# Performance work log

Measured on AMD Instinct MI355X. Metric: run time of the kernel, lower is better.

The kernel has to match this reference:

```python
import jax, jax.numpy as jnp
import numpy as np

N = 4096
IN_F = 256
OUT_F = 64
K = 4
ALPHA = 0.2  # LeakyReLU negative slope
NEG_INF = -9e15


def setup_inputs() -> dict:
    key = jax.random.key(0)
    k_h, k_w, k_a, k_e, k_m = jax.random.split(key, 5)
    h = jax.random.normal(k_h, (N, IN_F), dtype=jnp.float32)
    # xavier_uniform with gain=1.414
    def xavier(k, shape, gain=1.414):
        fan_in, fan_out = shape[0], shape[1]
        limit = gain * np.sqrt(6.0 / (fan_in + fan_out))
        return jax.random.uniform(k, shape, jnp.float32, -limit, limit)
    W = xavier(k_w, (IN_F, OUT_F))
    a = xavier(k_a, (2 * OUT_F, 1))
    vals = jax.random.uniform(k_e, (K, N, N), dtype=jnp.float32)
    mask = jax.random.uniform(k_m, (K, N, N), dtype=jnp.float32) < 0.05
    edge_attr = jnp.where(mask, vals, 0.0)
    return {"h": h, "edge_attr": edge_attr, "W": W, "a": a}


def reference(h, edge_attr, W, a):
    # h: [N, IN_F], edge_attr: [K, N, N], W: [IN_F, OUT_F], a: [2*OUT_F, 1]
    Wh = h @ W                                   # [N, OUT_F]
    Wh1 = Wh @ a[:OUT_F, :]                      # [N, 1]
    Wh2 = Wh @ a[OUT_F:, :]                      # [N, 1]
    e = jax.nn.leaky_relu(Wh1 + Wh2.T, negative_slope=ALPHA)  # [N, N]
    e = e[None, :, :] * edge_attr                # [K, N, N]
    e = jnp.where(edge_attr > 0, e, NEG_INF)
    att = jax.nn.softmax(e, axis=1)              # softmax over dim=1, as in torch
    # dropout is identity in eval mode
    # batched replacement for the per-channel python loop of matmuls
    hp = jnp.einsum('kij,jf->kif', att, Wh)      # [K, N, OUT_F]
    out = jnp.transpose(hp, (1, 0, 2)).reshape(N, K * OUT_F)  # concat dim=1
    return jax.nn.elu(out), att
```

## Files before the change

kernel.cpp:

```cpp
#include <hip/hip_runtime.h>

#define NN 4096
#define IN_F 256
#define OUT_F 64
#define K_CH 4
#define ALPHA 0.2f
#define ROWS1 32
#define IC1 128
#define BSTRIDE 264

typedef __bf16 bf16;
typedef __attribute__((ext_vector_type(8))) __bf16 bf16x8;
typedef __attribute__((ext_vector_type(4))) __bf16 bf16x4;
typedef __attribute__((ext_vector_type(4))) float f32x4;

__global__ __launch_bounds__(256) void k0_wh(const float* __restrict__ h,
                                             const float* __restrict__ W,
                                             const float* __restrict__ a,
                                             float* __restrict__ Wh,
                                             float* __restrict__ Wh1,
                                             float* __restrict__ Wh2) {
    int tid = threadIdx.x;
    int wave = tid >> 6, lane = tid & 63;
    int i = blockIdx.x * 4 + wave;
    const float* hrow = h + (size_t)i * IN_F;
    float acc = 0.f;
    #pragma unroll 8
    for (int c = 0; c < IN_F; ++c)
        acc += hrow[c] * W[c * OUT_F + lane];
    Wh[(size_t)i * OUT_F + lane] = acc;
    float v1 = acc * a[lane];
    float v2 = acc * a[OUT_F + lane];
    #pragma unroll
    for (int o = 32; o > 0; o >>= 1) {
        v1 += __shfl_xor(v1, o, 64);
        v2 += __shfl_xor(v2, o, 64);
    }
    if (lane == 0) { Wh1[i] = v1; Wh2[i] = v2; }
}

__global__ __launch_bounds__(256) void k0_transpose(const float* __restrict__ Wh,
                                                    bf16* __restrict__ WhT) {
    __shared__ float lds[OUT_F * 65];
    int tid = threadIdx.x;
    int i0 = blockIdx.x * 64;
    int f = tid & 63;
    int r0 = tid >> 6;
    #pragma unroll
    for (int s = 0; s < 16; ++s) {
        int r = r0 * 16 + s;
        lds[f * 65 + r] = Wh[(size_t)(i0 + r) * OUT_F + f];
    }
    __syncthreads();
    int f2 = tid >> 2;
    int c0 = (tid & 3) * 16;
    #pragma unroll
    for (int s = 0; s < 16; ++s) {
        int c = c0 + s;
        WhT[(size_t)f2 * NN + i0 + c] = (bf16)lds[f2 * 65 + c];
    }
}

__global__ __launch_bounds__(256) void k1_colsum(const float* __restrict__ edge,
                                                 const float* __restrict__ Wh1,
                                                 const float* __restrict__ Wh2,
                                                 bf16* __restrict__ p_buf,
                                                 float* __restrict__ partial) {
    int tid = threadIdx.x;
    int kch = blockIdx.z;
    int j0 = blockIdx.y * 1024 + tid * 4;
    int ic = blockIdx.x;
    int ibase = ic * ROWS1;
    f32x4 w2 = *(const f32x4*)&Wh2[j0];
    f32x4 w1v[ROWS1 / 4];
    #pragma unroll
    for (int t = 0; t < ROWS1 / 4; ++t)
        w1v[t] = *(const f32x4*)&Wh1[ibase + t * 4];
    f32x4 s = {0.f, 0.f, 0.f, 0.f};
    const float* base = edge + ((size_t)kch * NN + ibase) * NN + j0;
    bf16* pbase = p_buf + ((size_t)kch * NN + ibase) * NN + j0;
    f32x4 r[8];
    #pragma unroll
    for (int t = 0; t < 8; ++t)
        r[t] = __builtin_nontemporal_load((const f32x4*)(base + (size_t)t * NN));
    #pragma unroll
    for (int ii = 0; ii < ROWS1; ++ii) {
        int cur = ii & 7;
        f32x4 e = r[cur];
        int ip = (ii + 8 < ROWS1) ? ii + 8 : ii;
        r[cur] = __builtin_nontemporal_load((const f32x4*)(base + (size_t)ip * NN));
        float wh1 = w1v[ii >> 2][ii & 3];
        bf16x4 pv;
        #pragma unroll
        for (int c = 0; c < 4; ++c) {
            float xv = wh1 + w2[c];
            float lk = xv > 0.f ? xv : ALPHA * xv;
            float val = e[c] > 0.f ? __expf(lk * e[c]) : 0.f;
            bf16 vb = (bf16)val;
            pv[c] = vb;
            s[c] += (float)vb;
        }
        *(bf16x4*)(pbase + (size_t)ii * NN) = pv;
    }
    *(f32x4*)(partial + ((size_t)kch * IC1 + ic) * NN + j0) = s;
}

__global__ __launch_bounds__(256) void k1_reduce(const float* __restrict__ partial,
                                                 float* __restrict__ s_inv) {
    __shared__ float red[256];
    int tid = threadIdx.x;
    int kch = blockIdx.y;
    int jl = tid & 63, g = tid >> 6;
    int j = blockIdx.x * 64 + jl;
    const float* pb = partial + (size_t)kch * IC1 * NN;
    float s = 0.f;
    #pragma unroll 8
    for (int t = 0; t < IC1 / 4; ++t)
        s += pb[(size_t)(g * (IC1 / 4) + t) * NN + j];
    red[tid] = s;
    __syncthreads();
    if (tid < 64) {
        float tot = red[tid] + red[tid + 64] + red[tid + 128] + red[tid + 192];
        s_inv[kch * NN + j] = tot > 0.f ? 1.f / tot : 0.f;
    }
}

__global__ __launch_bounds__(256) void k2_fused(const bf16* __restrict__ p_buf,
                                                const float* __restrict__ s_inv,
                                                const bf16* __restrict__ WhT,
                                                float* __restrict__ att_out,
                                                float* __restrict__ out) {
    __shared__ bf16 ldsB[OUT_F * BSTRIDE];
    __shared__ float lds_inv[NN];
    int tid = threadIdx.x;
    int itile = blockIdx.x;
    int kch = blockIdx.y;
    #pragma unroll
    for (int t = 0; t < NN / 256; ++t)
        lds_inv[t * 256 + tid] = s_inv[kch * NN + t * 256 + tid];
    int wave = tid >> 6, lane = tid & 63;
    int n16 = lane & 15, quad = lane >> 4;
    int i_row = itile * 64 + wave * 16 + n16;
    const size_t ebase = ((size_t)kch * NN + i_row) * NN + quad * 8;
    const bf16* pptr = p_buf + ebase;
    float* aptr = att_out + ebase;
    f32x4 acc[4] = {};
    bf16x8 pf[8];
    #pragma unroll
    for (int t = 0; t < 8; ++t)
        pf[t] = *(const bf16x8*)(pptr + t * 32);
    int f = tid >> 2, part = (tid & 3) * 64;
    const bf16* wsrc = WhT + (size_t)f * NN + part;
    for (int slab = 0; slab < 16; ++slab) {
        __syncthreads();
        #pragma unroll
        for (int u = 0; u < 8; ++u) {
            bf16x8 v = *(const bf16x8*)(wsrc + slab * 256 + u * 8);
            *(bf16x8*)&ldsB[f * BSTRIDE + part + u * 8] = v;
        }
        __syncthreads();
        #pragma unroll
        for (int t = 0; t < 8; ++t) {
            int g = slab * 8 + t;
            int cur = g & 7;
            bf16x8 pv = pf[cur];
            int gp = (g + 8 < 128) ? g + 8 : g;
            pf[cur] = *(const bf16x8*)(pptr + gp * 32);
            int jg = g * 32 + quad * 8;
            int jl = t * 32 + quad * 8;
            f32x4 iv0 = *(const f32x4*)&lds_inv[jg];
            f32x4 iv1 = *(const f32x4*)&lds_inv[jg + 4];
            bf16x8 afrag;
            f32x4 av0, av1;
            #pragma unroll
            for (int c = 0; c < 8; ++c) {
                float isc = c < 4 ? iv0[c] : iv1[c - 4];
                float attv = (float)pv[c] * isc;
                afrag[c] = (bf16)attv;
                if (c < 4) av0[c] = attv; else av1[c - 4] = attv;
            }
            *(f32x4*)(aptr + g * 32) = av0;
            *(f32x4*)(aptr + g * 32 + 4) = av1;
            #pragma unroll
            for (int ft = 0; ft < 4; ++ft) {
                bf16x8 bfrag = *(const bf16x8*)&ldsB[(ft * 16 + n16) * BSTRIDE + jl];
                acc[ft] = __builtin_amdgcn_mfma_f32_16x16x32_bf16(afrag, bfrag, acc[ft], 0, 0, 0);
            }
        }
    }
    #pragma unroll
    for (int ft = 0; ft < 4; ++ft) {
        #pragma unroll
        for (int r = 0; r < 4; ++r) {
            int row_l = quad * 4 + r;
            int i_g = itile * 64 + wave * 16 + row_l;
            float v = acc[ft][r];
            out[(size_t)i_g * (K_CH * OUT_F) + kch * OUT_F + ft * 16 + n16] =
                v > 0.f ? v : __expf(v) - 1.f;
        }
    }
}

extern "C" void kernel_launch(void* const* d_in, const int* in_sizes, int n_in,
                              void* d_out, int out_size, void* d_ws, size_t ws_size,
                              hipStream_t stream) {
    (void)out_size; (void)ws_size;
    const float *h = nullptr, *edge = nullptr, *W = nullptr, *a = nullptr;
    for (int i = 0; i < n_in; ++i) {
        int sz = in_sizes[i];
        if (sz == NN * IN_F)               h    = (const float*)d_in[i];
        else if (sz == K_CH * NN * NN)     edge = (const float*)d_in[i];
        else if (sz == IN_F * OUT_F)       W    = (const float*)d_in[i];
        else if (sz == 2 * OUT_F)          a    = (const float*)d_in[i];
    }

    char* ws = (char*)d_ws;
    size_t off = 0;
    float* Wh      = (float*)(ws + off); off += (size_t)NN * OUT_F * 4;
    float* Wh1     = (float*)(ws + off); off += NN * 4;
    float* Wh2     = (float*)(ws + off); off += NN * 4;
    float* s_inv   = (float*)(ws + off); off += (size_t)K_CH * NN * 4;
    bf16*  WhT     = (bf16*) (ws + off); off += (size_t)OUT_F * NN * 2;
    float* partial = (float*)(ws + off); off += (size_t)K_CH * IC1 * NN * 4;
    bf16*  p_buf   = (bf16*) (ws + off); off += (size_t)K_CH * NN * NN * 2;

    float* out_h   = (float*)d_out;
    float* att_out = out_h + (size_t)NN * (K_CH * OUT_F);

    k0_wh<<<dim3(NN / 4), 256, 0, stream>>>(h, W, a, Wh, Wh1, Wh2);
    k0_transpose<<<dim3(NN / 64), 256, 0, stream>>>(Wh, WhT);
    k1_colsum<<<dim3(IC1, 4, K_CH), 256, 0, stream>>>(edge, Wh1, Wh2, p_buf, partial);
    k1_reduce<<<dim3(NN / 64, K_CH), 256, 0, stream>>>(partial, s_inv);
    k2_fused<<<dim3(64, K_CH), 256, 0, stream>>>(p_buf, s_inv, WhT, att_out, out_h);
}
```

Measured before the change: 565.0 us.

## Fold column normalization into per-channel scaled Wh and split attention write kernel

The column softmax scale is now applied to Wh (producing a per-channel scaled WhTs in the reduce kernel) so the MFMA kernel feeds unnormalized p directly, and the fp32 attention output is written by a separate wide elementwise kernel with nontemporal loads and stores. This removes per-element scaling and the large attention stores from the low-occupancy MFMA kernel (256 blocks), so the bandwidth-heavy att write can use many more blocks. In exchange p_buf is read twice, and the rounding of the product changes slightly. The transpose store is also vectorized.

Result: no change. 565.2 us (+0.0%).

```diff
diff --git a/kernel.cpp b/kernel.cpp
--- a/kernel.cpp
+++ b/kernel.cpp
@@ -54,11 +54,14 @@
     __syncthreads();
     int f2 = tid >> 2;
     int c0 = (tid & 3) * 16;
-    #pragma unroll
-    for (int s = 0; s < 16; ++s) {
-        int c = c0 + s;
-        WhT[(size_t)f2 * NN + i0 + c] = (bf16)lds[f2 * 65 + c];
-    }
+    bf16x8 v0, v1;
+    #pragma unroll
+    for (int s = 0; s < 8; ++s) {
+        v0[s] = (bf16)lds[f2 * 65 + c0 + s];
+        v1[s] = (bf16)lds[f2 * 65 + c0 + 8 + s];
+    }
+    *(bf16x8*)&WhT[(size_t)f2 * NN + i0 + c0] = v0;
+    *(bf16x8*)&WhT[(size_t)f2 * NN + i0 + c0 + 8] = v1;
 }
 
 __global__ __launch_bounds__(256) void k1_colsum(const float* __restrict__ edge,
@@ -106,12 +109,16 @@
 }
 
 __global__ __launch_bounds__(256) void k1_reduce(const float* __restrict__ partial,
-                                                 float* __restrict__ s_inv) {
+                                                 const bf16* __restrict__ WhT,
+                                                 float* __restrict__ s_inv,
+                                                 bf16* __restrict__ WhTs) {
     __shared__ float red[256];
+    __shared__ float inv_l[64];
     int tid = threadIdx.x;
     int kch = blockIdx.y;
     int jl = tid & 63, g = tid >> 6;
-    int j = blockIdx.x * 64 + jl;
+    int jbase = blockIdx.x * 64;
+    int j = jbase + jl;
     const float* pb = partial + (size_t)kch * IC1 * NN;
     float s = 0.f;
     #pragma unroll 8
@@ -121,36 +128,44 @@
     __syncthreads();
     if (tid < 64) {
         float tot = red[tid] + red[tid + 64] + red[tid + 128] + red[tid + 192];
-        s_inv[kch * NN + j] = tot > 0.f ? 1.f / tot : 0.f;
-    }
-}
-
-__global__ __launch_bounds__(256) void k2_fused(const bf16* __restrict__ p_buf,
-                                                const float* __restrict__ s_inv,
-                                                const bf16* __restrict__ WhT,
-                                                float* __restrict__ att_out,
-                                                float* __restrict__ out) {
+        float iv = tot > 0.f ? 1.f / tot : 0.f;
+        s_inv[kch * NN + j] = iv;
+        inv_l[tid] = iv;
+    }
+    __syncthreads();
+    int f = tid >> 2;
+    int c0 = (tid & 3) * 16;
+    bf16x8 a0 = *(const bf16x8*)&WhT[(size_t)f * NN + jbase + c0];
+    bf16x8 a1 = *(const bf16x8*)&WhT[(size_t)f * NN + jbase + c0 + 8];
+    bf16x8 o0, o1;
+    #pragma unroll
+    for (int s2 = 0; s2 < 8; ++s2) {
+        o0[s2] = (bf16)((float)a0[s2] * inv_l[c0 + s2]);
+        o1[s2] = (bf16)((float)a1[s2] * inv_l[c0 + 8 + s2]);
+    }
+    bf16* wb = WhTs + ((size_t)kch * OUT_F + f) * NN + jbase + c0;
+    *(bf16x8*)wb = o0;
+    *(bf16x8*)(wb + 8) = o1;
+}
+
+__global__ __launch_bounds__(256) void k2_mfma(const bf16* __restrict__ p_buf,
+                                               const bf16* __restrict__ WhTs,
+                                               float* __restrict__ out) {
     __shared__ bf16 ldsB[OUT_F * BSTRIDE];
-    __shared__ float lds_inv[NN];
     int tid = threadIdx.x;
     int itile = blockIdx.x;
     int kch = blockIdx.y;
-    #pragma unroll
-    for (int t = 0; t < NN / 256; ++t)
-        lds_inv[t * 256 + tid] = s_inv[kch * NN + t * 256 + tid];
     int wave = tid >> 6, lane = tid & 63;
     int n16 = lane & 15, quad = lane >> 4;
     int i_row = itile * 64 + wave * 16 + n16;
-    const size_t ebase = ((size_t)kch * NN + i_row) * NN + quad * 8;
-    const bf16* pptr = p_buf + ebase;
-    float* aptr = att_out + ebase;
+    const bf16* pptr = p_buf + ((size_t)kch * NN + i_row) * NN + quad * 8;
     f32x4 acc[4] = {};
     bf16x8 pf[8];
     #pragma unroll
     for (int t = 0; t < 8; ++t)
-        pf[t] = *(const bf16x8*)(pptr + t * 32);
+        pf[t] = __builtin_nontemporal_load((const bf16x8*)(pptr + t * 32));
     int f = tid >> 2, part = (tid & 3) * 64;
-    const bf16* wsrc = WhT + (size_t)f * NN + part;
+    const bf16* wsrc = WhTs + ((size_t)kch * OUT_F + f) * NN + part;
     for (int slab = 0; slab < 16; ++slab) {
         __syncthreads();
         #pragma unroll
@@ -163,24 +178,10 @@
         for (int t = 0; t < 8; ++t) {
             int g = slab * 8 + t;
             int cur = g & 7;
-            bf16x8 pv = pf[cur];
+            bf16x8 afrag = pf[cur];
             int gp = (g + 8 < 128) ? g + 8 : g;
-            pf[cur] = *(const bf16x8*)(pptr + gp * 32);
-            int jg = g * 32 + quad * 8;
+            pf[cur] = __builtin_nontemporal_load((const bf16x8*)(pptr + gp * 32));
             int jl = t * 32 + quad * 8;
-            f32x4 iv0 = *(const f32x4*)&lds_inv[jg];
-            f32x4 iv1 = *(const f32x4*)&lds_inv[jg + 4];
-            bf16x8 afrag;
-            f32x4 av0, av1;
-            #pragma unroll
-            for (int c = 0; c < 8; ++c) {
-                float isc = c < 4 ? iv0[c] : iv1[c - 4];
-                float attv = (float)pv[c] * isc;
-                afrag[c] = (bf16)attv;
-                if (c < 4) av0[c] = attv; else av1[c - 4] = attv;
-            }
-            *(f32x4*)(aptr + g * 32) = av0;
-            *(f32x4*)(aptr + g * 32 + 4) = av1;
             #pragma unroll
             for (int ft = 0; ft < 4; ++ft) {
                 bf16x8 bfrag = *(const bf16x8*)&ldsB[(ft * 16 + n16) * BSTRIDE + jl];
@@ -198,6 +199,32 @@
             out[(size_t)i_g * (K_CH * OUT_F) + kch * OUT_F + ft * 16 + n16] =
                 v > 0.f ? v : __expf(v) - 1.f;
         }
+    }
+}
+
+__global__ __launch_bounds__(256) void k2_att(const bf16* __restrict__ p_buf,
+                                              const float* __restrict__ s_inv,
+                                              float* __restrict__ att_out) {
+    int kch = blockIdx.y;
+    const bf16* pb = p_buf + (size_t)kch * NN * NN;
+    float* ab = att_out + (size_t)kch * NN * NN;
+    const float* inv = s_inv + kch * NN;
+    #pragma unroll
+    for (int it = 0; it < 4; ++it) {
+        size_t chunk = ((size_t)it * 2048 + blockIdx.x) * 256 + threadIdx.x;
+        size_t base = chunk * 8;
+        int j0 = (int)(base & (NN - 1));
+        bf16x8 pv = __builtin_nontemporal_load((const bf16x8*)(pb + base));
+        f32x4 iv0 = *(const f32x4*)&inv[j0];
+        f32x4 iv1 = *(const f32x4*)&inv[j0 + 4];
+        f32x4 a0, a1;
+        #pragma unroll
+        for (int c = 0; c < 4; ++c) {
+            a0[c] = (float)pv[c] * iv0[c];
+            a1[c] = (float)pv[c + 4] * iv1[c];
+        }
+        __builtin_nontemporal_store(a0, (f32x4*)(ab + base));
+        __builtin_nontemporal_store(a1, (f32x4*)(ab + base + 4));
     }
 }
 
@@ -221,6 +248,7 @@
     float* Wh2     = (float*)(ws + off); off += NN * 4;
     float* s_inv   = (float*)(ws + off); off += (size_t)K_CH * NN * 4;
     bf16*  WhT     = (bf16*) (ws + off); off += (size_t)OUT_F * NN * 2;
+    bf16*  WhTs    = (bf16*) (ws + off); off += (size_t)K_CH * OUT_F * NN * 2;
     float* partial = (float*)(ws + off); off += (size_t)K_CH * IC1 * NN * 4;
     bf16*  p_buf   = (bf16*) (ws + off); off += (size_t)K_CH * NN * NN * 2;
 
@@ -230,6 +258,7 @@
     k0_wh<<<dim3(NN / 4), 256, 0, stream>>>(h, W, a, Wh, Wh1, Wh2);
     k0_transpose<<<dim3(NN / 64), 256, 0, stream>>>(Wh, WhT);
     k1_colsum<<<dim3(IC1, 4, K_CH), 256, 0, stream>>>(edge, Wh1, Wh2, p_buf, partial);
-    k1_reduce<<<dim3(NN / 64, K_CH), 256, 0, stream>>>(partial, s_inv);
-    k2_fused<<<dim3(64, K_CH), 256, 0, stream>>>(p_buf, s_inv, WhT, att_out, out_h);
-}
+    k1_reduce<<<dim3(NN / 64, K_CH), 256, 0, stream>>>(partial, WhT, s_inv, WhTs);
+    k2_mfma<<<dim3(64, K_CH), 256, 0, stream>>>(p_buf, WhTs, out_h);
+    k2_att<<<dim3(2048, K_CH), 256, 0, stream>>>(p_buf, s_inv, att_out);
+}
```
